# Optimization experiments

Measured on AMD Instinct MI355X. Metric: run time of the kernel, lower is better.

The kernel has to match this reference:

```python
import jax, jax.numpy as jnp
import numpy as np
from jax.scipy.special import erfinv

EMBED = 384
HEADS = 6
HEAD_DIM = EMBED // HEADS  # 64
N_FREQS = HEAD_DIM // 2    # 32
SEQ = 1025                 # 1 CLS + 32*32 patches
POS_DIM = 2
MIN_FREQ, MAX_FREQ = 0.1, 1000.0


def _phi(m: int) -> float:
    x = 2.0
    for _ in range(10):
        x = (1.0 + x) ** (1.0 / (m + 1.0))
    return x


def _uniform_directions(n: int, d: int) -> jnp.ndarray:
    # golden-ratio quasi-random directions, normalized (matches uniform_directions_jax)
    g = _phi(d)
    alpha = (1.0 / g) ** jnp.arange(1, d + 1, dtype=jnp.float32)
    i = jnp.arange(1, n + 1, dtype=jnp.float32)[:, None]
    z = jnp.fmod(i * alpha, 1.0)
    dirs = erfinv(2.0 * z - 1.0)
    return dirs / jnp.linalg.norm(dirs, axis=1, keepdims=True)


def _rope_freqs() -> jnp.ndarray:  # [h, F, P]
    omega = MIN_FREQ * (MAX_FREQ / MIN_FREQ) ** jnp.linspace(0.0, 1.0, N_FREQS)
    dirs = _uniform_directions(HEADS * N_FREQS, POS_DIM).reshape(HEADS, N_FREQS, POS_DIM)
    return dirs * omega.reshape(1, N_FREQS, 1)


def _coords_2d() -> jnp.ndarray:  # [S, 2], CLS at origin, patches in [-1,1]^2
    n = int(np.sqrt(SEQ - 1))  # 32
    yy, xx = jnp.meshgrid(jnp.arange(n), jnp.arange(n), indexing='ij')
    xf = xx.flatten().astype(jnp.float32) / (n - 1) * 2 - 1
    yf = yy.flatten().astype(jnp.float32) / (n - 1) * 2 - 1
    patch = jnp.stack([xf, yf], axis=1)
    return jnp.concatenate([jnp.zeros((1, 2), jnp.float32), patch], axis=0)


def _apply_rope(t_bshd, freqs_hFP, coords_SP):
    # theta: [S, h, F]
    theta = jnp.einsum('hfp,sp->shf', freqs_hFP, coords_SP)
    cos, sin = jnp.cos(theta), jnp.sin(theta)  # broadcast over batch
    x1, y1 = jnp.split(t_bshd, 2, axis=-1)     # [b,s,h,F] each
    return jnp.concatenate([x1 * cos - y1 * sin, x1 * sin + y1 * cos], axis=-1)


def setup_inputs() -> dict:
    key = jax.random.key(0)
    ks = jax.random.split(key, 6)
    scale = 1.0 / np.sqrt(EMBED)
    return {
        'x':  jax.random.normal(ks[0], (16, SEQ, EMBED), jnp.float32),
        'Wq': jax.random.normal(ks[1], (EMBED, EMBED), jnp.float32) * scale,
        'Wk': jax.random.normal(ks[2], (EMBED, EMBED), jnp.float32) * scale,
        'Wv': jax.random.normal(ks[3], (EMBED, EMBED), jnp.float32) * scale,
        'Wo': jax.random.normal(ks[4], (EMBED, EMBED), jnp.float32) * scale,
        'bo': jnp.zeros((EMBED,), jnp.float32),
    }


def reference(x, Wq, Wk, Wv, Wo, bo):
    b, s, e = x.shape
    freqs = _rope_freqs()   # constant buffers
    coords = _coords_2d()
    q = (x @ Wq).reshape(b, s, HEADS, HEAD_DIM)
    k = (x @ Wk).reshape(b, s, HEADS, HEAD_DIM)
    v = (x @ Wv).reshape(b, s, HEADS, HEAD_DIM)
    q = _apply_rope(q, freqs, coords)
    k = _apply_rope(k, freqs, coords)
    scores = jnp.einsum('blhd,bmhd->bhlm', q, k) / np.sqrt(HEAD_DIM)
    attn = jax.nn.softmax(scores, axis=-1)
    out = jnp.einsum('bhlm,bmhd->blhd', attn, v).reshape(b, s, e)
    return out @ Wo + bo
```

## Files before the change

kernel.cpp:

```cpp
#include <hip/hip_runtime.h>
#include <hip/hip_bf16.h>
#include <math.h>

#define EMBED 384
#define HEADS 6
#define HD    64
#define NF    32
#define SEQ   1025
#define SEQP  1088
#define BATCH 16
#define MTOT  (BATCH*SEQ)
#define NCHUNK 17
#define LSTRIDE 72
#define VSTR   68
#define GSTR 40

#define NB_X2B 6150
#define NB_TW  144
#define NB_RT  769

typedef __bf16 bf16x8 __attribute__((ext_vector_type(8)));
typedef __bf16 bf16x4 __attribute__((ext_vector_type(4)));
typedef float  f32x4  __attribute__((ext_vector_type(4)));
typedef short  s16x4  __attribute__((ext_vector_type(4)));

#define MFMA_BF16(A,B,C) __builtin_amdgcn_mfma_f32_16x16x32_bf16((A),(B),(C),0,0,0)
#define MFMA16(A,B,C) __builtin_amdgcn_mfma_f32_16x16x16bf16_1k((A),(B),(C),0,0,0)

__device__ __forceinline__ __bf16 f2bf(float f){
    __hip_bfloat16 h = __float2bfloat16(f);
    return *reinterpret_cast<__bf16*>(&h);
}
__device__ __forceinline__ short bfbits(float f){
    __hip_bfloat16 h = __float2bfloat16(f);
    return *reinterpret_cast<short*>(&h);
}

__device__ __forceinline__ float erfinv_f(float x){
    float w = -log1pf(-x*x);
    float p;
    if (w < 5.0f){
        w -= 2.5f;
        p = 2.81022636e-08f;
        p = fmaf(p, w, 3.43273939e-07f);
        p = fmaf(p, w, -3.5233877e-06f);
        p = fmaf(p, w, -4.39150654e-06f);
        p = fmaf(p, w, 0.00021858087f);
        p = fmaf(p, w, -0.00125372503f);
        p = fmaf(p, w, -0.00417768164f);
        p = fmaf(p, w, 0.246640727f);
        p = fmaf(p, w, 1.50140941f);
    } else {
        w = sqrtf(w) - 3.0f;
        p = -0.000200214257f;
        p = fmaf(p, w, 0.000100950558f);
        p = fmaf(p, w, 0.00134934322f);
        p = fmaf(p, w, -0.00367342844f);
        p = fmaf(p, w, 0.00573950773f);
        p = fmaf(p, w, -0.0076224613f);
        p = fmaf(p, w, 0.00943887047f);
        p = fmaf(p, w, 1.00167406f);
        p = fmaf(p, w, 2.83297682f);
    }
    return p * x;
}

__global__ __launch_bounds__(256) void prep_kernel(
    const float* __restrict__ x, __hip_bfloat16* __restrict__ xb,
    const float* __restrict__ Wq, const float* __restrict__ Wk,
    const float* __restrict__ Wv, const float* __restrict__ Wo,
    __hip_bfloat16* __restrict__ Wt,
    float* __restrict__ cos_t, float* __restrict__ sin_t)
{
    __shared__ float tile[64][65];
    const int bid = blockIdx.x;
    const int tid = threadIdx.x;

    if (bid < NB_X2B){
        int i = bid*256 + tid;
        float4 v = *reinterpret_cast<const float4*>(x + (size_t)i*4);
        bf16x4 b; b[0]=f2bf(v.x); b[1]=f2bf(v.y); b[2]=f2bf(v.z); b[3]=f2bf(v.w);
        *reinterpret_cast<bf16x4*>(reinterpret_cast<__bf16*>(xb) + (size_t)i*4) = b;
        return;
    }
    if (bid < NB_X2B + NB_TW){
        int idx = bid - NB_X2B;
        const int mat = idx / 36;
        const int rem = idx % 36;
        const int kx = rem / 6, ny = rem % 6;
        const float* W = (mat==0)?Wq:(mat==1)?Wk:(mat==2)?Wv:Wo;
        const int k0 = kx*64, n0 = ny*64;
        const int c = tid & 63, rq = tid >> 6;
        #pragma unroll
        for (int i = 0; i < 16; ++i){
            int row = rq*16 + i;
            tile[row][c] = W[(size_t)(k0+row)*EMBED + n0 + c];
        }
        __syncthreads();
        #pragma unroll
        for (int i = 0; i < 16; ++i){
            int nr = rq*16 + i;
            Wt[((size_t)mat*EMBED + n0 + nr)*EMBED + k0 + c] = __float2bfloat16(tile[c][nr]);
        }
        return;
    }
    int idx = (bid - NB_X2B - NB_TW)*256 + tid;
    if (idx >= SEQ*HEADS*NF) return;
    int f  = idx & (NF-1);
    int hf = idx / NF;
    int h  = hf % HEADS;
    int s  = hf / HEADS;

    double xd = 2.0;
    #pragma unroll
    for (int it = 0; it < 10; ++it) xd = cbrt(1.0 + xd);
    float a1 = (float)(1.0 / xd);
    float a2 = a1 * a1;

    float fi = (float)(h*NF + f + 1);
    float z1 = fmodf(fi * a1, 1.0f);
    float z2 = fmodf(fi * a2, 1.0f);
    float d1 = erfinv_f(2.0f*z1 - 1.0f);
    float d2 = erfinv_f(2.0f*z2 - 1.0f);
    float inv = 1.0f / sqrtf(d1*d1 + d2*d2);
    d1 *= inv; d2 *= inv;

    float omega = 0.1f * powf(10000.0f, (float)f / 31.0f);
    float fx = d1 * omega, fy = d2 * omega;

    float cx = 0.0f, cy = 0.0f;
    if (s > 0){
        int pi = s - 1;
        cx = (float)(pi & 31) / 31.0f * 2.0f - 1.0f;
        cy = (float)(pi >> 5) / 31.0f * 2.0f - 1.0f;
    }
    float theta = fx*cx + fy*cy;
    float sv, cv;
    sincosf(theta, &sv, &cv);
    cos_t[idx] = cv;
    sin_t[idx] = sv;
}

__global__ __launch_bounds__(256, 3) void qkv_rope_kernel(
    const __hip_bfloat16* __restrict__ xb_,
    const __hip_bfloat16* __restrict__ Wt,
    const float* __restrict__ cos_t,
    const float* __restrict__ sin_t,
    __hip_bfloat16* __restrict__ qbuf,
    __hip_bfloat16* __restrict__ kbuf,
    __hip_bfloat16* __restrict__ vbuf)
{
    __shared__ __align__(16) __bf16 xs[128*GSTR];
    __shared__ __align__(16) __bf16 bt[128*GSTR];
    const int tid = threadIdx.x;
    const int m0 = blockIdx.x * 128;
    const int j  = blockIdx.y;
    const __bf16* xb = reinterpret_cast<const __bf16*>(xb_);
    const __bf16* wt = reinterpret_cast<const __bf16*>(Wt);

    int soff[2], arow[2], brow[2];
    #pragma unroll
    for (int i = 0; i < 2; ++i){
        int g = tid + i*256;
        int row = g >> 2, kc = g & 3;
        soff[i] = row*GSTR + kc*8;
        int am = m0 + row; if (am > MTOT-1) am = MTOT-1;
        arow[i] = am;
        brow[i] = j*128 + row;
    }

    bf16x8 ar[2], br[2];
    #pragma unroll
    for (int i = 0; i < 2; ++i){
        int g = tid + i*256, kc = g & 3;
        ar[i] = *reinterpret_cast<const bf16x8*>(xb + (size_t)arow[i]*EMBED + kc*8);
        br[i] = *reinterpret_cast<const bf16x8*>(wt + (size_t)brow[i]*EMBED + kc*8);
    }

    const int w = tid >> 6;
    const int lane = tid & 63;
    const int quad = lane >> 4, low = lane & 15;
    const int mh = w >> 1, nh = w & 1;
    const int mw0 = m0 + mh*64;

    f32x4 acc[4][4] = {};
    for (int kb = 0; kb < 12; ++kb){
        __syncthreads();
        #pragma unroll
        for (int i = 0; i < 2; ++i){
            *reinterpret_cast<bf16x8*>(&xs[soff[i]]) = ar[i];
            *reinterpret_cast<bf16x8*>(&bt[soff[i]]) = br[i];
        }
        __syncthreads();
        if (kb < 11){
            const int k1 = (kb+1)*32;
            #pragma unroll
            for (int i = 0; i < 2; ++i){
                int g = tid + i*256, kc = g & 3;
                ar[i] = *reinterpret_cast<const bf16x8*>(xb + (size_t)arow[i]*EMBED + k1 + kc*8);
                br[i] = *reinterpret_cast<const bf16x8*>(wt + (size_t)brow[i]*EMBED + k1 + kc*8);
            }
        }
        bf16x8 af[4], bfr[4];
        #pragma unroll
        for (int mt = 0; mt < 4; ++mt)
            af[mt] = *reinterpret_cast<const bf16x8*>(&xs[(mh*64 + mt*16 + low)*GSTR + quad*8]);
        #pragma unroll
        for (int t = 0; t < 4; ++t)
            bfr[t] = *reinterpret_cast<const bf16x8*>(&bt[(nh*64 + t*16 + low)*GSTR + quad*8]);
        #pragma unroll
        for (int t = 0; t < 4; ++t)
            #pragma unroll
            for (int mt = 0; mt < 4; ++mt)
                acc[mt][t] = MFMA_BF16(af[mt], bfr[t], acc[mt][t]);
    }

    const int n64 = j*2 + nh;
    const int mat = n64 / 6;
    const int h   = n64 % 6;

    if (mat == 2){
        #pragma unroll
        for (int mt = 0; mt < 4; ++mt)
            #pragma unroll
            for (int t = 0; t < 4; ++t)
                #pragma unroll
                for (int r = 0; r < 4; ++r){
                    int m = mw0 + mt*16 + quad*4 + r;
                    if (m < MTOT){
                        int b = m / SEQ, s = m % SEQ;
                        vbuf[((size_t)(b*HEADS + h)*SEQ + s)*HD + t*16 + low] = __float2bfloat16(acc[mt][t][r]);
                    }
                }
    } else {
        __hip_bfloat16* ob = (mat == 0) ? qbuf : kbuf;
        const float qs_ = (mat == 0) ? 0.125f : 1.0f;
        #pragma unroll
        for (int mt = 0; mt < 4; ++mt)
            #pragma unroll
            for (int t = 0; t < 2; ++t)
                #pragma unroll
                for (int r = 0; r < 4; ++r){
                    int m = mw0 + mt*16 + quad*4 + r;
                    if (m < MTOT){
                        int b = m / SEQ, s = m % SEQ;
                        int f = t*16 + low;
                        float cv = cos_t[(s*HEADS + h)*NF + f];
                        float sv = sin_t[(s*HEADS + h)*NF + f];
                        float x1 = acc[mt][t][r];
                        float y1 = acc[mt][t+2][r];
                        size_t base = ((size_t)(b*HEADS + h)*SEQ + s)*HD;
                        ob[base + f]      = __float2bfloat16((x1*cv - y1*sv)*qs_);
                        ob[base + NF + f] = __float2bfloat16((x1*sv + y1*cv)*qs_);
                    }
                }
    }
}

__global__ __launch_bounds__(256) void vt_transpose_kernel(
    const __hip_bfloat16* __restrict__ v, __hip_bfloat16* __restrict__ vt)
{
    __shared__ __bf16 tileT[64*72];
    const int tid = threadIdx.x;
    const int bh = blockIdx.x;
    const int s0 = blockIdx.y * 64;
    const __bf16* vb = reinterpret_cast<const __bf16*>(v) + (size_t)bh*SEQ*HD;
    #pragma unroll
    for (int i = 0; i < 2; ++i){
        int ch = tid + i*256;
        int srow = ch >> 3, dg = ch & 7;
        int s = s0 + srow; if (s > SEQ-1) s = SEQ-1;
        bf16x8 val = *reinterpret_cast<const bf16x8*>(vb + (size_t)s*HD + dg*8);
        #pragma unroll
        for (int e = 0; e < 8; ++e)
            tileT[(dg*8 + e)*72 + srow] = val[e];
    }
    __syncthreads();
    __bf16* ot = reinterpret_cast<__bf16*>(vt) + (size_t)bh*HD*SEQP;
    #pragma unroll
    for (int i = 0; i < 2; ++i){
        int ch = tid + i*256;
        int d = ch >> 3, sg = ch & 7;
        bf16x8 val = *reinterpret_cast<const bf16x8*>(&tileT[d*72 + sg*8]);
        *reinterpret_cast<bf16x8*>(ot + (size_t)d*SEQP + s0 + sg*8) = val;
    }
}

__global__ __launch_bounds__(256, 4) void attn_kernel(
    const __hip_bfloat16* __restrict__ qbuf,
    const __hip_bfloat16* __restrict__ kbuf,
    const __hip_bfloat16* __restrict__ vtbuf,
    __hip_bfloat16* __restrict__ aout)
{
    __shared__ __align__(16) __bf16 kls[64*LSTRIDE];
    __shared__ __align__(16) __bf16 vls[64*VSTR];
    const int tid  = threadIdx.x;
    const int w    = tid >> 6;
    const int lane = tid & 63;
    const int quad = lane >> 4, low = lane & 15;
    const int id = blockIdx.x;
    const int bh = id % 96;
    const int qt = id / 96;
    const int b = bh / HEADS, h = bh % HEADS;
    const __bf16* qb = reinterpret_cast<const __bf16*>(qbuf);
    const __bf16* kb = reinterpret_cast<const __bf16*>(kbuf);
    const __bf16* vt = reinterpret_cast<const __bf16*>(vtbuf);
    const size_t base   = (size_t)bh * SEQ * HD;
    const size_t vtbase = (size_t)bh * HD * SEQP;
    const int q0 = qt*128 + w*32;

    int srow[2], sgk[2], soffk[2], soffv[2];
    #pragma unroll
    for (int i = 0; i < 2; ++i){
        int ch = tid + i*256;
        srow[i] = ch >> 3; sgk[i] = ch & 7;
        soffk[i] = srow[i]*LSTRIDE + sgk[i]*8;
        soffv[i] = srow[i]*VSTR    + sgk[i]*8;
    }

    bf16x8 bq[2][2];
    #pragma unroll
    for (int nt = 0; nt < 2; ++nt){
        int qs = q0 + nt*16 + low; if (qs > SEQ-1) qs = SEQ-1;
        #pragma unroll
        for (int ks = 0; ks < 2; ++ks)
            bq[nt][ks] = *reinterpret_cast<const bf16x8*>(qb + base + (size_t)qs*HD + ks*32 + quad*8);
    }

    bf16x8 kr[2], vr[2];
    #pragma unroll
    for (int i = 0; i < 2; ++i){
        int kk = srow[i]; if (kk > SEQ-1) kk = SEQ-1;
        kr[i] = *reinterpret_cast<const bf16x8*>(kb + base + (size_t)kk*HD + sgk[i]*8);
        vr[i] = *reinterpret_cast<const bf16x8*>(vt + vtbase + (size_t)srow[i]*SEQP + sgk[i]*8);
    }

    f32x4 o[2][4] = {};
    float l_i[2] = {0.f, 0.f};

    for (int c = 0; c < NCHUNK; ++c){
        const int c0 = c*64;
        __syncthreads();
        #pragma unroll
        for (int i = 0; i < 2; ++i){
            *reinterpret_cast<bf16x8*>(&kls[soffk[i]]) = kr[i];
            bf16x4 vlo = __builtin_shufflevector(vr[i], vr[i], 0,1,2,3);
            bf16x4 vhi = __builtin_shufflevector(vr[i], vr[i], 4,5,6,7);
            *reinterpret_cast<bf16x4*>(&vls[soffv[i]])     = vlo;
            *reinterpret_cast<bf16x4*>(&vls[soffv[i] + 4]) = vhi;
        }
        __syncthreads();
        if (c + 1 < NCHUNK){
            const int c1 = c0 + 64;
            #pragma unroll
            for (int i = 0; i < 2; ++i){
                int kk = c1 + srow[i]; if (kk > SEQ-1) kk = SEQ-1;
                kr[i] = *reinterpret_cast<const bf16x8*>(kb + base + (size_t)kk*HD + sgk[i]*8);
                vr[i] = *reinterpret_cast<const bf16x8*>(vt + vtbase + (size_t)srow[i]*SEQP + c1 + sgk[i]*8);
            }
        }
        f32x4 st[4][2] = {};
        #pragma unroll
        for (int kt = 0; kt < 4; ++kt)
            #pragma unroll
            for (int ks = 0; ks < 2; ++ks){
                bf16x8 ak = *reinterpret_cast<const bf16x8*>(&kls[(kt*16 + low)*LSTRIDE + ks*32 + quad*8]);
                #pragma unroll
                for (int nt = 0; nt < 2; ++nt)
                    st[kt][nt] = MFMA_BF16(ak, bq[nt][ks], st[kt][nt]);
            }
        if (c0 + 64 > SEQ){
            #pragma unroll
            for (int kt = 0; kt < 4; ++kt)
                #pragma unroll
                for (int r = 0; r < 4; ++r){
                    int key = c0 + kt*16 + quad*4 + r;
                    if (key >= SEQ){ st[kt][0][r] = -1e30f; st[kt][1][r] = -1e30f; }
                }
        }
        s16x4 pa[4][2];
        #pragma unroll
        for (int nt = 0; nt < 2; ++nt)
            #pragma unroll
            for (int kt = 0; kt < 4; ++kt)
                #pragma unroll
                for (int r = 0; r < 4; ++r){
                    float p = __expf(st[kt][nt][r]);
                    l_i[nt] += p;
                    pa[kt][nt][r] = bfbits(p);
                }
        #pragma unroll
        for (int kt = 0; kt < 4; ++kt)
            #pragma unroll
            for (int dt = 0; dt < 4; ++dt){
                const s16x4 bv = *reinterpret_cast<const s16x4*>(&vls[(dt*16 + low)*VSTR + kt*16 + quad*4]);
                #pragma unroll
                for (int nt = 0; nt < 2; ++nt)
                    o[nt][dt] = MFMA16(pa[kt][nt], bv, o[nt][dt]);
            }
    }

    #pragma unroll
    for (int nt = 0; nt < 2; ++nt){
        l_i[nt] += __shfl_xor(l_i[nt], 16, 64);
        l_i[nt] += __shfl_xor(l_i[nt], 32, 64);
    }
    float lq[2][4];
    #pragma unroll
    for (int nt = 0; nt < 2; ++nt)
        #pragma unroll
        for (int r = 0; r < 4; ++r)
            lq[nt][r] = __shfl(l_i[nt], quad*4 + r, 64);

    #pragma unroll
    for (int nt = 0; nt < 2; ++nt)
        #pragma unroll
        for (int r = 0; r < 4; ++r){
            int s = q0 + nt*16 + quad*4 + r;
            if (s < SEQ){
                float inv = 1.0f / lq[nt][r];
                __hip_bfloat16* dst = aout + ((size_t)b*SEQ + s)*EMBED + h*HD;
                #pragma unroll
                for (int dt = 0; dt < 4; ++dt)
                    dst[dt*16 + low] = __float2bfloat16(o[nt][dt][r]*inv);
            }
        }
}

__global__ __launch_bounds__(256, 3) void outproj_kernel(
    const __hip_bfloat16* __restrict__ a,
    const __hip_bfloat16* __restrict__ Wt,
    const float* __restrict__ bo,
    float* __restrict__ out)
{
    __shared__ __align__(16) __bf16 xs[128*GSTR];
    __shared__ __align__(16) __bf16 bt[128*GSTR];
    const int tid = threadIdx.x;
    const int m0 = blockIdx.x * 128;
    const int j  = blockIdx.y;
    const __bf16* ab = reinterpret_cast<const __bf16*>(a);
    const __bf16* wt = reinterpret_cast<const __bf16*>(Wt) + (size_t)3*EMBED*EMBED;

    int soff[2], arow[2], brow[2];
    #pragma unroll
    for (int i = 0; i < 2; ++i){
        int g = tid + i*256;
        int row = g >> 2, kc = g & 3;
        soff[i] = row*GSTR + kc*8;
        int am = m0 + row; if (am > MTOT-1) am = MTOT-1;
        arow[i] = am;
        brow[i] = j*128 + row;
    }
    bf16x8 ar[2], br[2];
    #pragma unroll
    for (int i = 0; i < 2; ++i){
        int g = tid + i*256, kc = g & 3;
        ar[i] = *reinterpret_cast<const bf16x8*>(ab + (size_t)arow[i]*EMBED + kc*8);
        br[i] = *reinterpret_cast<const bf16x8*>(wt + (size_t)brow[i]*EMBED + kc*8);
    }

    const int w = tid >> 6;
    const int lane = tid & 63;
    const int quad = lane >> 4, low = lane & 15;
    const int mh = w >> 1, nh = w & 1;
    const int mw0 = m0 + mh*64;
    const int n0 = j*128 + nh*64;

    f32x4 acc[4][4] = {};
    for (int kb = 0; kb < 12; ++kb){
        __syncthreads();
        #pragma unroll
        for (int i = 0; i < 2; ++i){
            *reinterpret_cast<bf16x8*>(&xs[soff[i]]) = ar[i];
            *reinterpret_cast<bf16x8*>(&bt[soff[i]]) = br[i];
        }
        __syncthreads();
        if (kb < 11){
            const int k1 = (kb+1)*32;
            #pragma unroll
            for (int i = 0; i < 2; ++i){
                int g = tid + i*256, kc = g & 3;
                ar[i] = *reinterpret_cast<const bf16x8*>(ab + (size_t)arow[i]*EMBED + k1 + kc*8);
                br[i] = *reinterpret_cast<const bf16x8*>(wt + (size_t)brow[i]*EMBED + k1 + kc*8);
            }
        }
        bf16x8 af[4], bfr[4];
        #pragma unroll
        for (int mt = 0; mt < 4; ++mt)
            af[mt] = *reinterpret_cast<const bf16x8*>(&xs[(mh*64 + mt*16 + low)*GSTR + quad*8]);
        #pragma unroll
        for (int t = 0; t < 4; ++t)
            bfr[t] = *reinterpret_cast<const bf16x8*>(&bt[(nh*64 + t*16 + low)*GSTR + quad*8]);
        #pragma unroll
        for (int t = 0; t < 4; ++t)
            #pragma unroll
            for (int mt = 0; mt < 4; ++mt)
                acc[mt][t] = MFMA_BF16(af[mt], bfr[t], acc[mt][t]);
    }

    #pragma unroll
    for (int t = 0; t < 4; ++t){
        const int n = n0 + t*16 + low;
        const float bias = bo[n];
        #pragma unroll
        for (int mt = 0; mt < 4; ++mt)
            #pragma unroll
            for (int r = 0; r < 4; ++r){
                const int m = mw0 + mt*16 + quad*4 + r;
                if (m < MTOT) out[(size_t)m*EMBED + n] = acc[mt][t][r] + bias;
            }
    }
}

extern "C" void kernel_launch(void* const* d_in, const int* in_sizes, int n_in,
                              void* d_out, int out_size, void* d_ws, size_t ws_size,
                              hipStream_t stream)
{
    const float* x  = (const float*)d_in[0];
    const float* Wq = (const float*)d_in[1];
    const float* Wk = (const float*)d_in[2];
    const float* Wv = (const float*)d_in[3];
    const float* Wo = (const float*)d_in[4];
    const float* bo = (const float*)d_in[5];
    float* out = (float*)d_out;

    const size_t NE = (size_t)MTOT * EMBED;
    const size_t VT = (size_t)BATCH*HEADS*HD*SEQP;
    char* ws = (char*)d_ws;
    size_t off = 0;
    __hip_bfloat16* qbuf = (__hip_bfloat16*)(ws + off); off += 2*NE;
    __hip_bfloat16* kbuf = (__hip_bfloat16*)(ws + off); off += 2*NE;
    __hip_bfloat16* abuf = (__hip_bfloat16*)(ws + off); off += 2*NE;
    __hip_bfloat16* vbuf = (__hip_bfloat16*)(ws + off); off += 2*NE;
    __hip_bfloat16* xbuf = (__hip_bfloat16*)(ws + off); off += 2*NE;
    __hip_bfloat16* vt   = (__hip_bfloat16*)(ws + off); off += 2*VT;
    __hip_bfloat16* Wt   = (__hip_bfloat16*)(ws + off); off += (size_t)4*EMBED*EMBED*2;
    float* cos_t = (float*)(ws + off); off += (size_t)SEQ*HEADS*NF*4;
    float* sin_t = (float*)(ws + off); off += (size_t)SEQ*HEADS*NF*4;

    prep_kernel<<<dim3(NB_X2B + NB_TW + NB_RT), dim3(256), 0, stream>>>(
        x, xbuf, Wq, Wk, Wv, Wo, Wt, cos_t, sin_t);
    qkv_rope_kernel<<<dim3((MTOT + 127)/128, 9), dim3(256), 0, stream>>>(xbuf, Wt, cos_t, sin_t, qbuf, kbuf, vbuf);
    vt_transpose_kernel<<<dim3(96, 17), dim3(256), 0, stream>>>(vbuf, vt);
    attn_kernel<<<dim3(864), dim3(256), 0, stream>>>(qbuf, kbuf, vt, abuf);
    outproj_kernel<<<dim3((MTOT + 127)/128, 3), dim3(256), 0, stream>>>(abuf, Wt, bo, out);
}
```

Before: 206.5 us.

## Drop LDS staging in attention, use single-wave blocks with XCD-aware mapping

```diff
diff --git a/kernel.cpp b/kernel.cpp
--- a/kernel.cpp
+++ b/kernel.cpp
@@ -11,8 +11,6 @@
 #define BATCH 16
 #define MTOT  (BATCH*SEQ)
 #define NCHUNK 17
-#define LSTRIDE 72
-#define VSTR   68
 #define GSTR 40
 
 #define NB_X2B 6150
@@ -234,7 +232,7 @@
                 }
     } else {
         __hip_bfloat16* ob = (mat == 0) ? qbuf : kbuf;
-        const float qs_ = (mat == 0) ? 0.125f : 1.0f;
+        const float qs_ = (mat == 0) ? 0.125f*1.44269504088896340736f : 1.0f;
         #pragma unroll
         for (int mt = 0; mt < 4; ++mt)
             #pragma unroll
@@ -286,37 +284,25 @@
     }
 }
 
-__global__ __launch_bounds__(256, 4) void attn_kernel(
+__global__ __launch_bounds__(64) void attn_kernel(
     const __hip_bfloat16* __restrict__ qbuf,
     const __hip_bfloat16* __restrict__ kbuf,
     const __hip_bfloat16* __restrict__ vtbuf,
     __hip_bfloat16* __restrict__ aout)
 {
-    __shared__ __align__(16) __bf16 kls[64*LSTRIDE];
-    __shared__ __align__(16) __bf16 vls[64*VSTR];
-    const int tid  = threadIdx.x;
-    const int w    = tid >> 6;
-    const int lane = tid & 63;
+    const int lane = threadIdx.x;
     const int quad = lane >> 4, low = lane & 15;
     const int id = blockIdx.x;
-    const int bh = id % 96;
-    const int qt = id / 96;
+    const int xcd = id & 7, slot = id >> 3;
+    const int bh = xcd*12 + slot/36;
+    const int j  = slot % 36;
+    const int qt = j >> 2, w = j & 3;
     const int b = bh / HEADS, h = bh % HEADS;
     const __bf16* qb = reinterpret_cast<const __bf16*>(qbuf);
-    const __bf16* kb = reinterpret_cast<const __bf16*>(kbuf);
-    const __bf16* vt = reinterpret_cast<const __bf16*>(vtbuf);
-    const size_t base   = (size_t)bh * SEQ * HD;
-    const size_t vtbase = (size_t)bh * HD * SEQP;
+    const __bf16* kb = reinterpret_cast<const __bf16*>(kbuf) + (size_t)bh*SEQ*HD;
+    const __bf16* vt = reinterpret_cast<const __bf16*>(vtbuf) + (size_t)bh*HD*SEQP;
+    const size_t base = (size_t)bh * SEQ * HD;
     const int q0 = qt*128 + w*32;
-
-    int srow[2], sgk[2], soffk[2], soffv[2];
-    #pragma unroll
-    for (int i = 0; i < 2; ++i){
-        int ch = tid + i*256;
-        srow[i] = ch >> 3; sgk[i] = ch & 7;
-        soffk[i] = srow[i]*LSTRIDE + sgk[i]*8;
-        soffv[i] = srow[i]*VSTR    + sgk[i]*8;
-    }
 
     bf16x8 bq[2][2];
     #pragma unroll
@@ -327,48 +313,26 @@
             bq[nt][ks] = *reinterpret_cast<const bf16x8*>(qb + base + (size_t)qs*HD + ks*32 + quad*8);
     }
 
-    bf16x8 kr[2], vr[2];
-    #pragma unroll
-    for (int i = 0; i < 2; ++i){
-        int kk = srow[i]; if (kk > SEQ-1) kk = SEQ-1;
-        kr[i] = *reinterpret_cast<const bf16x8*>(kb + base + (size_t)kk*HD + sgk[i]*8);
-        vr[i] = *reinterpret_cast<const bf16x8*>(vt + vtbase + (size_t)srow[i]*SEQP + sgk[i]*8);
-    }
-
     f32x4 o[2][4] = {};
     float l_i[2] = {0.f, 0.f};
 
     for (int c = 0; c < NCHUNK; ++c){
         const int c0 = c*64;
-        __syncthreads();
-        #pragma unroll
-        for (int i = 0; i < 2; ++i){
-            *reinterpret_cast<bf16x8*>(&kls[soffk[i]]) = kr[i];
-            bf16x4 vlo = __builtin_shufflevector(vr[i], vr[i], 0,1,2,3);
-            bf16x4 vhi = __builtin_shufflevector(vr[i], vr[i], 4,5,6,7);
-            *reinterpret_cast<bf16x4*>(&vls[soffv[i]])     = vlo;
-            *reinterpret_cast<bf16x4*>(&vls[soffv[i] + 4]) = vhi;
-        }
-        __syncthreads();
-        if (c + 1 < NCHUNK){
-            const int c1 = c0 + 64;
-            #pragma unroll
-            for (int i = 0; i < 2; ++i){
-                int kk = c1 + srow[i]; if (kk > SEQ-1) kk = SEQ-1;
-                kr[i] = *reinterpret_cast<const bf16x8*>(kb + base + (size_t)kk*HD + sgk[i]*8);
-                vr[i] = *reinterpret_cast<const bf16x8*>(vt + vtbase + (size_t)srow[i]*SEQP + c1 + sgk[i]*8);
+        f32x4 st[4][2] = {};
+        #pragma unroll
+        for (int ks = 0; ks < 2; ++ks){
+            bf16x8 ak[4];
+            #pragma unroll
+            for (int kt = 0; kt < 4; ++kt){
+                int kk = c0 + kt*16 + low; if (kk > SEQ-1) kk = SEQ-1;
+                ak[kt] = *reinterpret_cast<const bf16x8*>(kb + (size_t)kk*HD + ks*32 + quad*8);
             }
-        }
-        f32x4 st[4][2] = {};
-        #pragma unroll
-        for (int kt = 0; kt < 4; ++kt)
-            #pragma unroll
-            for (int ks = 0; ks < 2; ++ks){
-                bf16x8 ak = *reinterpret_cast<const bf16x8*>(&kls[(kt*16 + low)*LSTRIDE + ks*32 + quad*8]);
+            #pragma unroll
+            for (int kt = 0; kt < 4; ++kt)
                 #pragma unroll
                 for (int nt = 0; nt < 2; ++nt)
-                    st[kt][nt] = MFMA_BF16(ak, bq[nt][ks], st[kt][nt]);
-            }
+                    st[kt][nt] = MFMA_BF16(ak[kt], bq[nt][ks], st[kt][nt]);
+        }
         if (c0 + 64 > SEQ){
             #pragma unroll
             for (int kt = 0; kt < 4; ++kt)
@@ -385,19 +349,27 @@
             for (int kt = 0; kt < 4; ++kt)
                 #pragma unroll
                 for (int r = 0; r < 4; ++r){
-                    float p = __expf(st[kt][nt][r]);
+                    float p = exp2f(st[kt][nt][r]);
                     l_i[nt] += p;
                     pa[kt][nt][r] = bfbits(p);
                 }
         #pragma unroll
-        for (int kt = 0; kt < 4; ++kt)
-            #pragma unroll
-            for (int dt = 0; dt < 4; ++dt){
-                const s16x4 bv = *reinterpret_cast<const s16x4*>(&vls[(dt*16 + low)*VSTR + kt*16 + quad*4]);
-                #pragma unroll
-                for (int nt = 0; nt < 2; ++nt)
-                    o[nt][dt] = MFMA16(pa[kt][nt], bv, o[nt][dt]);
-            }
+        for (int kp = 0; kp < 2; ++kp){
+            s16x4 bv[2][4];
+            #pragma unroll
+            for (int ki = 0; ki < 2; ++ki)
+                #pragma unroll
+                for (int dt = 0; dt < 4; ++dt)
+                    bv[ki][dt] = *reinterpret_cast<const s16x4*>(
+                        vt + (size_t)(dt*16 + low)*SEQP + c0 + (kp*2+ki)*16 + quad*4);
+            #pragma unroll
+            for (int ki = 0; ki < 2; ++ki)
+                #pragma unroll
+                for (int dt = 0; dt < 4; ++dt)
+                    #pragma unroll
+                    for (int nt = 0; nt < 2; ++nt)
+                        o[nt][dt] = MFMA16(pa[kp*2+ki][nt], bv[ki][dt], o[nt][dt]);
+        }
     }
 
     #pragma unroll
@@ -542,6 +514,6 @@
         x, xbuf, Wq, Wk, Wv, Wo, Wt, cos_t, sin_t);
     qkv_rope_kernel<<<dim3((MTOT + 127)/128, 9), dim3(256), 0, stream>>>(xbuf, Wt, cos_t, sin_t, qbuf, kbuf, vbuf);
     vt_transpose_kernel<<<dim3(96, 17), dim3(256), 0, stream>>>(vbuf, vt);
-    attn_kernel<<<dim3(864), dim3(256), 0, stream>>>(qbuf, kbuf, vt, abuf);
+    attn_kernel<<<dim3(3456), dim3(64), 0, stream>>>(qbuf, kbuf, vt, abuf);
     outproj_kernel<<<dim3((MTOT + 127)/128, 3), dim3(256), 0, stream>>>(abuf, Wt, bo, out);
 }
```

Measured after the change: 338.5 us. 1.64x slower.
